# Optimization experiments

Hardware: AMD Instinct MI355X
Metric: run time of the kernel (lower is better)

The kernel has to match this reference:

```python
import jax, jax.numpy as jnp
import numpy as np

HEAD_DIM = 128
KS = 3          # kernel_size
DIL = 1         # dilation
SCALE = HEAD_DIM ** (-0.5)  # qk_scale defaults to head_dim**-0.5


def _unfold(x, ks, dil):
    # Equivalent of nn.Unfold(ks, dil, pad=dil*(ks-1)//2, stride=1), reshaped to
    # [B, d, ks*ks, H, W] (torch's C-major-then-kernel ordering matches stacking
    # kernel offsets on a new axis after the channel axis).
    B, d, H, W = x.shape
    p = dil * (ks - 1) // 2
    xp = jnp.pad(x, ((0, 0), (0, 0), (p, p), (p, p)))
    patches = [xp[:, :, i * dil:i * dil + H, j * dil:j * dil + W]
               for i in range(ks) for j in range(ks)]
    return jnp.stack(patches, axis=2)  # [B, d, ks*ks, H, W]


def setup_inputs() -> dict:
    key = jax.random.key(0)
    k1, k2, k3 = jax.random.split(key, 3)
    shape = (32, HEAD_DIM, 64, 64)
    return {
        "q": jax.random.normal(k1, shape, dtype=jnp.float32),
        "k": jax.random.normal(k2, shape, dtype=jnp.float32),
        "v": jax.random.normal(k3, shape, dtype=jnp.float32),
    }


def reference(q, k, v):
    # Local (unfold) branch: dilation=1 < 5.
    kk = _unfold(k, KS, DIL)                                   # [B,d,9,H,W]
    logits = jnp.einsum('bdhw,bdkhw->bkhw', q, kk) * SCALE     # per-pixel q @ k_window
    attn = jax.nn.softmax(logits, axis=1)                      # softmax over 9 neighbors
    vv = _unfold(v, KS, DIL)                                   # [B,d,9,H,W]
    x = jnp.einsum('bkhw,bdkhw->bhwd', attn, vv)               # [B,H,W,d]
    return x
```

## Files before the change

kernel.cpp:

```cpp
#include <hip/hip_runtime.h>

static constexpr int HD   = 128;
static constexpr int HH   = 64;
static constexpr int WW   = 64;
static constexpr int ROWS = 2;
static constexpr int BLK  = 512;
static constexpr int HALO = ROWS + 2;
static constexpr int DC   = 16;
static constexpr int NCH  = HD / DC;
static constexpr int LSTR = 20;
static constexpr float SCALE = 0.08838834764831845f;

__global__ __launch_bounds__(BLK, 4) void natten3_kernel(
    const float* __restrict__ Q, const float* __restrict__ K,
    const float* __restrict__ V, float* __restrict__ O)
{
  __shared__ float buf[2][HALO * WW * LSTR];

  const int tid = threadIdx.x;
  const int qf  = tid & 3;
  const int px  = tid >> 2;
  const int w   = px & 63;
  const int pr  = px >> 6;

  const int bid = blockIdx.x;
  const int swz = (bid & 7) * 128 + (bid >> 3);
  const int b   = swz >> 5;
  const int h0  = (swz & 31) * ROWS;
  const int hh  = h0 + pr;

  const int plane = HH * WW;
  const size_t img = (size_t)HD * plane;
  const float* Qb = Q + (size_t)b * img;
  const float* Kb = K + (size_t)b * img;
  const float* Vb = V + (size_t)b * img;
  const int qoff = hh * WW + w;
  const int dq   = 4 * qf;

  int sg_g[2], sg_l[2];
  #pragma unroll
  for (int it = 0; it < 2; ++it) {
    const int idx  = it * BLK + tid;
    const int ws   = idx & 63;
    const int rest = idx >> 6;
    const int is   = rest >> 2;
    const int gs   = rest & 3;
    const int grow = min(max(h0 - 1 + is, 0), HH - 1);
    sg_g[it] = gs * 4 * plane + grow * WW + ws;
    sg_l[it] = (is * WW + ws) * LSTR + gs * 4;
  }

  int   lofs[9];
  float msk[9];
  #pragma unroll
  for (int dh = 0; dh < 3; ++dh) {
    #pragma unroll
    for (int dw = 0; dw < 3; ++dw) {
      const int j = dh * 3 + dw;
      const int r = hh + dh - 1, c = w + dw - 1;
      msk[j] = (r >= 0 && r < HH && c >= 0 && c < WW) ? 1.0f : 0.0f;
      const int cc = min(max(c, 0), WW - 1);
      lofs[j] = ((pr + dh) * WW + cc) * LSTR + dq;
    }
  }

  {
    float s[2][4];
    #pragma unroll
    for (int it = 0; it < 2; ++it)
      #pragma unroll
      for (int p = 0; p < 4; ++p)
        s[it][p] = Kb[sg_g[it] + p * plane];
    #pragma unroll
    for (int it = 0; it < 2; ++it)
      *(float4*)&buf[0][sg_l[it]] = make_float4(s[it][0], s[it][1], s[it][2], s[it][3]);
  }
  float q[4];
  #pragma unroll
  for (int p = 0; p < 4; ++p) q[p] = Qb[(dq + p) * plane + qoff];
  __syncthreads();

  float logit[9];
  #pragma unroll
  for (int j = 0; j < 9; ++j) logit[j] = 0.0f;

  for (int c = 0; c < NCH; ++c) {
    const int cur = c & 1;
    float s[2][4], qn[4];
    if (c + 1 < NCH) {
      const int dbase = (c + 1) * DC * plane;
      #pragma unroll
      for (int it = 0; it < 2; ++it)
        #pragma unroll
        for (int p = 0; p < 4; ++p)
          s[it][p] = Kb[dbase + sg_g[it] + p * plane];
      #pragma unroll
      for (int p = 0; p < 4; ++p)
        qn[p] = Qb[((c + 1) * DC + dq + p) * plane + qoff];
    }
    const float* __restrict__ bc = buf[cur];
    #pragma unroll
    for (int j = 0; j < 9; ++j) {
      const float4 k4 = *(const float4*)&bc[lofs[j]];
      float acc = logit[j];
      acc = fmaf(q[0], k4.x, acc); acc = fmaf(q[1], k4.y, acc);
      acc = fmaf(q[2], k4.z, acc); acc = fmaf(q[3], k4.w, acc);
      logit[j] = acc;
    }
    if (c + 1 < NCH) {
      #pragma unroll
      for (int it = 0; it < 2; ++it)
        *(float4*)&buf[cur ^ 1][sg_l[it]] = make_float4(s[it][0], s[it][1], s[it][2], s[it][3]);
      #pragma unroll
      for (int p = 0; p < 4; ++p) q[p] = qn[p];
    }
    __syncthreads();
  }

  float vs[2][4];
  #pragma unroll
  for (int it = 0; it < 2; ++it)
    #pragma unroll
    for (int p = 0; p < 4; ++p)
      vs[it][p] = Vb[sg_g[it] + p * plane];

  #pragma unroll
  for (int j = 0; j < 9; ++j) {
    logit[j] += __shfl_xor(logit[j], 1);
    logit[j] += __shfl_xor(logit[j], 2);
  }
  #pragma unroll
  for (int j = 0; j < 9; ++j) logit[j] = msk[j] * logit[j] * SCALE;
  float m = logit[0];
  #pragma unroll
  for (int j = 1; j < 9; ++j) m = fmaxf(m, logit[j]);
  float att[9];
  float Z = 0.0f;
  #pragma unroll
  for (int j = 0; j < 9; ++j) { att[j] = __expf(logit[j] - m); Z += att[j]; }
  const float rZ = 1.0f / Z;
  #pragma unroll
  for (int j = 0; j < 9; ++j) att[j] *= rZ * msk[j];

  #pragma unroll
  for (int it = 0; it < 2; ++it)
    *(float4*)&buf[0][sg_l[it]] = make_float4(vs[it][0], vs[it][1], vs[it][2], vs[it][3]);
  __syncthreads();

  const size_t obase = ((size_t)b * plane + (size_t)h0 * WW) * HD;
  float oprev[4];
  for (int c = 0; c < NCH; ++c) {
    const int cur = c & 1;
    float s[2][4];
    if (c + 1 < NCH) {
      const int dbase = (c + 1) * DC * plane;
      #pragma unroll
      for (int it = 0; it < 2; ++it)
        #pragma unroll
        for (int p = 0; p < 4; ++p)
          s[it][p] = Vb[dbase + sg_g[it] + p * plane];
    }
    float o0 = 0.f, o1 = 0.f, o2 = 0.f, o3 = 0.f;
    const float* __restrict__ bc = buf[cur];
    #pragma unroll
    for (int j = 0; j < 9; ++j) {
      const float4 v4 = *(const float4*)&bc[lofs[j]];
      const float a = att[j];
      o0 = fmaf(a, v4.x, o0); o1 = fmaf(a, v4.y, o1);
      o2 = fmaf(a, v4.z, o2); o3 = fmaf(a, v4.w, o3);
    }
    if (c & 1) {
      const size_t oa = obase + (size_t)px * HD + (size_t)(c - 1) * DC + dq;
      *(float4*)&O[oa]      = make_float4(oprev[0], oprev[1], oprev[2], oprev[3]);
      *(float4*)&O[oa + DC] = make_float4(o0, o1, o2, o3);
    } else {
      oprev[0] = o0; oprev[1] = o1; oprev[2] = o2; oprev[3] = o3;
    }
    if (c + 1 < NCH) {
      #pragma unroll
      for (int it = 0; it < 2; ++it)
        *(float4*)&buf[cur ^ 1][sg_l[it]] = make_float4(s[it][0], s[it][1], s[it][2], s[it][3]);
      __syncthreads();
    }
  }
}

extern "C" void kernel_launch(void* const* d_in, const int* in_sizes, int n_in,
                              void* d_out, int out_size, void* d_ws, size_t ws_size,
                              hipStream_t stream) {
  const float* q = (const float*)d_in[0];
  const float* k = (const float*)d_in[1];
  const float* v = (const float*)d_in[2];
  float* o = (float*)d_out;
  const int nblocks = 32 * (HH / ROWS);
  natten3_kernel<<<dim3(nblocks), dim3(BLK), 0, stream>>>(q, k, v, o);
}
```

Before: 46.56 us.

## Deepen K/V prefetch to two chunks, swizzle LDS layout, raise occupancy target

K and V chunk loads are now issued two chunks ahead using register ring buffers, and Q uses a three-deep rotation. Both chunk loops are fully unrolled so buffer indices resolve at compile time. The padded LDS stride of 20 is replaced by a dense stride of 16 with an XOR swizzle on the float4 slot, which shrinks shared memory per block while still avoiding bank conflicts. The launch bound is raised from 4 to 8, and the boundary mask is computed only at softmax time to cut register pressure. The goal is to hide more global-load latency in this memory-bound kernel. The cost is extra registers for the deeper prefetch, which could cause spills under the tighter occupancy bound.

```diff
diff --git a/kernel.cpp b/kernel.cpp
--- a/kernel.cpp
+++ b/kernel.cpp
@@ -8,10 +8,10 @@
 static constexpr int HALO = ROWS + 2;
 static constexpr int DC   = 16;
 static constexpr int NCH  = HD / DC;
-static constexpr int LSTR = 20;
+static constexpr int LSTR = 16;
 static constexpr float SCALE = 0.08838834764831845f;
 
-__global__ __launch_bounds__(BLK, 4) void natten3_kernel(
+__global__ __launch_bounds__(BLK, 8) void natten3_kernel(
     const float* __restrict__ Q, const float* __restrict__ K,
     const float* __restrict__ V, float* __restrict__ O)
 {
@@ -47,118 +47,140 @@
     const int gs   = rest & 3;
     const int grow = min(max(h0 - 1 + is, 0), HH - 1);
     sg_g[it] = gs * 4 * plane + grow * WW + ws;
-    sg_l[it] = (is * WW + ws) * LSTR + gs * 4;
-  }
-
-  int   lofs[9];
-  float msk[9];
+    sg_l[it] = (is * WW + ws) * LSTR + 4 * (gs ^ ((ws >> 2) & 3));
+  }
+
+  int lofs[9];
   #pragma unroll
   for (int dh = 0; dh < 3; ++dh) {
     #pragma unroll
     for (int dw = 0; dw < 3; ++dw) {
-      const int j = dh * 3 + dw;
-      const int r = hh + dh - 1, c = w + dw - 1;
-      msk[j] = (r >= 0 && r < HH && c >= 0 && c < WW) ? 1.0f : 0.0f;
-      const int cc = min(max(c, 0), WW - 1);
-      lofs[j] = ((pr + dh) * WW + cc) * LSTR + dq;
+      const int j  = dh * 3 + dw;
+      const int cc = min(max(w + dw - 1, 0), WW - 1);
+      lofs[j] = ((pr + dh) * WW + cc) * LSTR + 4 * (qf ^ ((cc >> 2) & 3));
     }
   }
 
   {
-    float s[2][4];
+    float s0[2][4];
     #pragma unroll
     for (int it = 0; it < 2; ++it)
       #pragma unroll
       for (int p = 0; p < 4; ++p)
-        s[it][p] = Kb[sg_g[it] + p * plane];
+        s0[it][p] = Kb[sg_g[it] + p * plane];
     #pragma unroll
     for (int it = 0; it < 2; ++it)
-      *(float4*)&buf[0][sg_l[it]] = make_float4(s[it][0], s[it][1], s[it][2], s[it][3]);
-  }
-  float q[4];
-  #pragma unroll
-  for (int p = 0; p < 4; ++p) q[p] = Qb[(dq + p) * plane + qoff];
+      *(float4*)&buf[0][sg_l[it]] = make_float4(s0[it][0], s0[it][1], s0[it][2], s0[it][3]);
+  }
+  float s[2][2][4];
+  #pragma unroll
+  for (int it = 0; it < 2; ++it)
+    #pragma unroll
+    for (int p = 0; p < 4; ++p)
+      s[1][it][p] = Kb[DC * plane + sg_g[it] + p * plane];
+  float q[3][4];
+  #pragma unroll
+  for (int p = 0; p < 4; ++p) q[0][p] = Qb[(dq + p) * plane + qoff];
+  #pragma unroll
+  for (int p = 0; p < 4; ++p) q[1][p] = Qb[(DC + dq + p) * plane + qoff];
   __syncthreads();
 
   float logit[9];
   #pragma unroll
   for (int j = 0; j < 9; ++j) logit[j] = 0.0f;
 
+  #pragma unroll
   for (int c = 0; c < NCH; ++c) {
     const int cur = c & 1;
-    float s[2][4], qn[4];
-    if (c + 1 < NCH) {
-      const int dbase = (c + 1) * DC * plane;
+    if (c + 2 < NCH) {
+      const int dbase = (c + 2) * DC * plane;
       #pragma unroll
       for (int it = 0; it < 2; ++it)
         #pragma unroll
         for (int p = 0; p < 4; ++p)
-          s[it][p] = Kb[dbase + sg_g[it] + p * plane];
+          s[cur][it][p] = Kb[dbase + sg_g[it] + p * plane];
       #pragma unroll
       for (int p = 0; p < 4; ++p)
-        qn[p] = Qb[((c + 1) * DC + dq + p) * plane + qoff];
+        q[(c + 2) % 3][p] = Qb[((c + 2) * DC + dq + p) * plane + qoff];
     }
     const float* __restrict__ bc = buf[cur];
+    const float* __restrict__ qc = q[c % 3];
     #pragma unroll
     for (int j = 0; j < 9; ++j) {
       const float4 k4 = *(const float4*)&bc[lofs[j]];
       float acc = logit[j];
-      acc = fmaf(q[0], k4.x, acc); acc = fmaf(q[1], k4.y, acc);
-      acc = fmaf(q[2], k4.z, acc); acc = fmaf(q[3], k4.w, acc);
+      acc = fmaf(qc[0], k4.x, acc); acc = fmaf(qc[1], k4.y, acc);
+      acc = fmaf(qc[2], k4.z, acc); acc = fmaf(qc[3], k4.w, acc);
       logit[j] = acc;
     }
     if (c + 1 < NCH) {
       #pragma unroll
       for (int it = 0; it < 2; ++it)
-        *(float4*)&buf[cur ^ 1][sg_l[it]] = make_float4(s[it][0], s[it][1], s[it][2], s[it][3]);
-      #pragma unroll
-      for (int p = 0; p < 4; ++p) q[p] = qn[p];
+        *(float4*)&buf[cur ^ 1][sg_l[it]] =
+            make_float4(s[(c + 1) & 1][it][0], s[(c + 1) & 1][it][1],
+                        s[(c + 1) & 1][it][2], s[(c + 1) & 1][it][3]);
     }
     __syncthreads();
   }
 
-  float vs[2][4];
+  float v[2][2][4];
   #pragma unroll
   for (int it = 0; it < 2; ++it)
     #pragma unroll
     for (int p = 0; p < 4; ++p)
-      vs[it][p] = Vb[sg_g[it] + p * plane];
+      v[0][it][p] = Vb[sg_g[it] + p * plane];
+  #pragma unroll
+  for (int it = 0; it < 2; ++it)
+    #pragma unroll
+    for (int p = 0; p < 4; ++p)
+      v[1][it][p] = Vb[DC * plane + sg_g[it] + p * plane];
 
   #pragma unroll
   for (int j = 0; j < 9; ++j) {
     logit[j] += __shfl_xor(logit[j], 1);
     logit[j] += __shfl_xor(logit[j], 2);
   }
-  #pragma unroll
-  for (int j = 0; j < 9; ++j) logit[j] = msk[j] * logit[j] * SCALE;
-  float m = logit[0];
-  #pragma unroll
-  for (int j = 1; j < 9; ++j) m = fmaxf(m, logit[j]);
   float att[9];
   float Z = 0.0f;
-  #pragma unroll
-  for (int j = 0; j < 9; ++j) { att[j] = __expf(logit[j] - m); Z += att[j]; }
-  const float rZ = 1.0f / Z;
-  #pragma unroll
-  for (int j = 0; j < 9; ++j) att[j] *= rZ * msk[j];
-
-  #pragma unroll
-  for (int it = 0; it < 2; ++it)
-    *(float4*)&buf[0][sg_l[it]] = make_float4(vs[it][0], vs[it][1], vs[it][2], vs[it][3]);
+  {
+    float msk[9];
+    #pragma unroll
+    for (int dh = 0; dh < 3; ++dh)
+      #pragma unroll
+      for (int dw = 0; dw < 3; ++dw) {
+        const int j = dh * 3 + dw;
+        const int r = hh + dh - 1, c = w + dw - 1;
+        msk[j] = (r >= 0 && r < HH && c >= 0 && c < WW) ? 1.0f : 0.0f;
+      }
+    #pragma unroll
+    for (int j = 0; j < 9; ++j) logit[j] = msk[j] * logit[j] * SCALE;
+    float m = logit[0];
+    #pragma unroll
+    for (int j = 1; j < 9; ++j) m = fmaxf(m, logit[j]);
+    #pragma unroll
+    for (int j = 0; j < 9; ++j) { att[j] = __expf(logit[j] - m); Z += att[j]; }
+    const float rZ = 1.0f / Z;
+    #pragma unroll
+    for (int j = 0; j < 9; ++j) att[j] *= rZ * msk[j];
+  }
+
+  #pragma unroll
+  for (int it = 0; it < 2; ++it)
+    *(float4*)&buf[0][sg_l[it]] = make_float4(v[0][it][0], v[0][it][1], v[0][it][2], v[0][it][3]);
   __syncthreads();
 
   const size_t obase = ((size_t)b * plane + (size_t)h0 * WW) * HD;
   float oprev[4];
+  #pragma unroll
   for (int c = 0; c < NCH; ++c) {
     const int cur = c & 1;
-    float s[2][4];
-    if (c + 1 < NCH) {
-      const int dbase = (c + 1) * DC * plane;
+    if (c + 2 < NCH) {
+      const int dbase = (c + 2) * DC * plane;
       #pragma unroll
       for (int it = 0; it < 2; ++it)
         #pragma unroll
         for (int p = 0; p < 4; ++p)
-          s[it][p] = Vb[dbase + sg_g[it] + p * plane];
+          v[cur][it][p] = Vb[dbase + sg_g[it] + p * plane];
     }
     float o0 = 0.f, o1 = 0.f, o2 = 0.f, o3 = 0.f;
     const float* __restrict__ bc = buf[cur];
@@ -179,7 +201,9 @@
     if (c + 1 < NCH) {
       #pragma unroll
       for (int it = 0; it < 2; ++it)
-        *(float4*)&buf[cur ^ 1][sg_l[it]] = make_float4(s[it][0], s[it][1], s[it][2], s[it][3]);
+        *(float4*)&buf[cur ^ 1][sg_l[it]] =
+            make_float4(v[(c + 1) & 1][it][0], v[(c + 1) & 1][it][1],
+                        v[(c + 1) & 1][it][2], v[(c + 1) & 1][it][3]);
       __syncthreads();
     }
   }
```

Measured after the change: 61.38 us. +31.8%, slower.
